# Kernel tuning notes

Hardware: AMD Instinct MI355X
Metric: run time of the kernel (lower is better)

## Reference

```python
import jax, jax.numpy as jnp
import numpy as np

B, S, D, H, E, TOPK = 4, 2048, 1024, 1024, 8, 2

def setup_inputs() -> dict:
    key = jax.random.key(0)
    k1, k2, k3 = jax.random.split(key, 3)
    x = jax.random.normal(k1, (B, S, D), dtype=jnp.float32)
    Wg = jax.random.normal(k2, (D, E), dtype=jnp.float32) * (1.0 / np.sqrt(D))
    bg = jnp.zeros((E,), dtype=jnp.float32)
    We = jax.random.normal(k3, (E, D, H), dtype=jnp.float32) * (1.0 / np.sqrt(D))
    be = jnp.zeros((E, H), dtype=jnp.float32)
    return {"x": x, "Wg": Wg, "bg": bg, "We": We, "be": be, "k": TOPK}

def reference(x, Wg, bg, We, be, k):
    # gate logits: [B, S, E]
    logits = jnp.einsum('bsd,de->bse', x, Wg) + bg
    # top-k gating (values, indices along expert axis)
    top_vals, sel = jax.lax.top_k(logits, k)            # [B, S, k]
    weights = jax.nn.softmax(top_vals.astype(jnp.float32), axis=-1).astype(x.dtype)
    # per-token combine weight for each expert: [B, S, E]
    onehot = jax.nn.one_hot(sel, E, dtype=x.dtype)      # [B, S, k, E]
    comb = jnp.einsum('bsk,bske->bse', weights, onehot)
    # all-expert dense outputs (equivalent math to per-expert gather+GEMM+scatter)
    y = jnp.einsum('bsd,edh->besh', x, We) + be[None, :, None, :]  # [B, E, S, H]
    out = jnp.einsum('bse,besh->bsh', comb, y)          # [B, S, H]
    return out
```

## Files before the change

### kernel.cpp

```cpp
#include <hip/hip_runtime.h>
#include <hip/hip_bf16.h>
#include <hip/hip_fp16.h>

#define NTOK 8192
#define DDIM 1024
#define HDIM 1024
#define NEXP 8

typedef __attribute__((ext_vector_type(8))) short short8;
typedef __attribute__((ext_vector_type(4))) float f32x4;
typedef __attribute__((ext_vector_type(4))) unsigned short us4;

static __device__ __forceinline__ unsigned short f2bf(float f) {
  union { float f; unsigned u; } v; v.f = f;
  return (unsigned short)((v.u + 0x7fffu + ((v.u >> 16) & 1u)) >> 16);
}

static __device__ __forceinline__ void gload16(const void* g, void* l) {
  __builtin_amdgcn_global_load_lds(
      (const __attribute__((address_space(1))) unsigned int*)g,
      (__attribute__((address_space(3))) unsigned int*)l, 16, 0, 0);
}

__global__ __launch_bounds__(256) void gate_kernel(
    const float* __restrict__ x, const float* __restrict__ Wg,
    const float* __restrict__ bg, unsigned short* __restrict__ xb,
    int* __restrict__ sel, float* __restrict__ wts)
{
  const int token = blockIdx.x * 4 + (threadIdx.x >> 6);
  const int lane = threadIdx.x & 63;
  const float* xr = x + (size_t)token * DDIM;

  float acc[NEXP];
#pragma unroll
  for (int e = 0; e < NEXP; ++e) acc[e] = 0.f;

#pragma unroll
  for (int q = 0; q < 4; ++q) {
    const int d0 = q * 256 + lane * 4;
    const float4 xv = *(const float4*)(xr + d0);
    us4 hb;
    hb.x = f2bf(xv.x); hb.y = f2bf(xv.y); hb.z = f2bf(xv.z); hb.w = f2bf(xv.w);
    *(us4*)(xb + (size_t)token * DDIM + d0) = hb;
    const float xs[4] = {xv.x, xv.y, xv.z, xv.w};
#pragma unroll
    for (int j = 0; j < 4; ++j) {
      const float* wr = Wg + (size_t)(d0 + j) * NEXP;
      const float4 wa = *(const float4*)wr;
      const float4 wb = *(const float4*)(wr + 4);
      acc[0] += xs[j] * wa.x; acc[1] += xs[j] * wa.y;
      acc[2] += xs[j] * wa.z; acc[3] += xs[j] * wa.w;
      acc[4] += xs[j] * wb.x; acc[5] += xs[j] * wb.y;
      acc[6] += xs[j] * wb.z; acc[7] += xs[j] * wb.w;
    }
  }

#pragma unroll
  for (int e = 0; e < NEXP; ++e) {
#pragma unroll
    for (int off = 32; off >= 1; off >>= 1)
      acc[e] += __shfl_xor(acc[e], off, 64);
  }

  if (lane == 0) {
    float v[NEXP];
#pragma unroll
    for (int e = 0; e < NEXP; ++e) v[e] = acc[e] + bg[e];
    int i0 = 0; float v0 = v[0];
#pragma unroll
    for (int e = 1; e < NEXP; ++e) if (v[e] > v0) { v0 = v[e]; i0 = e; }
    int i1 = -1; float v1 = -3.4e38f;
#pragma unroll
    for (int e = 0; e < NEXP; ++e) if (e != i0 && v[e] > v1) { v1 = v[e]; i1 = e; }
    const float t = __expf(v1 - v0);
    const float w0 = 1.f / (1.f + t);
    const float w1 = t / (1.f + t);
    sel[token * 2 + 0] = i0;  wts[token * 2 + 0] = w0;
    sel[token * 2 + 1] = i1;  wts[token * 2 + 1] = w1;
  }
}

__global__ __launch_bounds__(256) void route_kernel(
    const int* __restrict__ sel, const float* __restrict__ wts,
    int* __restrict__ counts, int* __restrict__ tlist, float* __restrict__ wlist,
    int* __restrict__ dstrow)
{
  __shared__ int bin[NEXP];
  __shared__ int base[NEXP];
  const int tid = threadIdx.x;
  if (tid < NEXP) bin[tid] = 0;
  __syncthreads();
  const int idx = blockIdx.x * 256 + tid;
  const int e = sel[idx];
  const float w = wts[idx];
  const int rank = atomicAdd(&bin[e], 1);
  __syncthreads();
  if (tid < NEXP) base[tid] = atomicAdd(&counts[tid], bin[tid]);
  __syncthreads();
  const int pos = base[e] + rank;
  tlist[e * NTOK + pos] = idx >> 1;
  wlist[e * NTOK + pos] = w;
  dstrow[e * NTOK + pos] = idx;
}

__global__ __launch_bounds__(256) void transpose_we(
    const float* __restrict__ We, unsigned short* __restrict__ wbt)
{
  const int e = blockIdx.z;
  const int h0 = blockIdx.x * 64;
  const int d0 = blockIdx.y * 64;
  __shared__ float t[64][65];
  const int tx = threadIdx.x;
  const int r0 = tx >> 4;
  const int c0 = (tx & 15) * 4;
  const float* src = We + ((size_t)e * DDIM + d0) * HDIM + h0;
#pragma unroll
  for (int i = 0; i < 4; ++i) {
    const int r = r0 + i * 16;
    const float4 v = *(const float4*)(src + (size_t)r * HDIM + c0);
    t[r][c0] = v.x; t[r][c0 + 1] = v.y; t[r][c0 + 2] = v.z; t[r][c0 + 3] = v.w;
  }
  __syncthreads();
#pragma unroll
  for (int i = 0; i < 4; ++i) {
    const int hr = r0 + i * 16;
    us4 o;
    o.x = f2bf(t[c0][hr]);
    o.y = f2bf(t[c0 + 1][hr]);
    o.z = f2bf(t[c0 + 2][hr]);
    o.w = f2bf(t[c0 + 3][hr]);
    *(us4*)(wbt + ((size_t)e * HDIM + h0 + hr) * DDIM + d0 + c0) = o;
  }
}

__global__ __launch_bounds__(512, 4) void moe_gemm(
    const unsigned short* __restrict__ xb,
    const unsigned short* __restrict__ wbt,
    const float* __restrict__ be,
    const int* __restrict__ counts,
    const int* __restrict__ tlist,
    const float* __restrict__ wlist,
    const int* __restrict__ dstrow,
    __half* __restrict__ yb)
{
  const int e = blockIdx.z;
  const int cnt = counts[e];
  const int tile = blockIdx.y;
  if (tile * 256 >= cnt) return;
  const int n0 = blockIdx.x * 128;

  __shared__ unsigned short As[256 * 64];
  __shared__ unsigned short Bs[128 * 64];

  const int tid = threadIdx.x;
  const int lane = tid & 63;
  const int wv = tid >> 6;
  const int wm = wv >> 1;
  const int wn = wv & 1;

  const int rA = tid >> 3;
  const int kbA = (tid & 7) << 4;
  int aOff[4]; int bOff[2]; int ldsA[4]; int ldsB[2];
#pragma unroll
  for (int q = 0; q < 4; ++q) {
    const int r = q * 64 + rA;
    int trow = tile * 256 + r;
    trow = trow < cnt ? trow : cnt - 1;
    const int tok = tlist[e * NTOK + trow];
    const int kbs = kbA ^ ((r & 7) << 4);
    aOff[q] = tok * DDIM + (kbs >> 1);
    ldsA[q] = r * 64 + (kbA >> 1);
  }
#pragma unroll
  for (int q = 0; q < 2; ++q) {
    const int r = q * 64 + rA;
    const int kbs = kbA ^ ((r & 7) << 4);
    bOff[q] = (e * HDIM + n0 + r) * DDIM + (kbs >> 1);
    ldsB[q] = r * 64 + (kbA >> 1);
  }

  f32x4 acc[4][4];
#pragma unroll
  for (int m = 0; m < 4; ++m)
#pragma unroll
    for (int n = 0; n < 4; ++n)
      acc[m][n] = (f32x4){0.f, 0.f, 0.f, 0.f};

  for (int kt = 0; kt < DDIM / 64; ++kt) {
    __syncthreads();
#pragma unroll
    for (int q = 0; q < 4; ++q) gload16(xb + aOff[q] + kt * 64, &As[ldsA[q]]);
#pragma unroll
    for (int q = 0; q < 2; ++q) gload16(wbt + bOff[q] + kt * 64, &Bs[ldsB[q]]);
    __syncthreads();

#pragma unroll
    for (int kk = 0; kk < 2; ++kk) {
      const int kb = kk * 64 + ((lane >> 4) << 4);
      short8 af[4], bfr[4];
#pragma unroll
      for (int m = 0; m < 4; ++m) {
        const int r = wm * 64 + m * 16 + (lane & 15);
        af[m] = *(const short8*)((const char*)As + r * 128 + (kb ^ ((r & 7) << 4)));
      }
#pragma unroll
      for (int n = 0; n < 4; ++n) {
        const int r = wn * 64 + n * 16 + (lane & 15);
        bfr[n] = *(const short8*)((const char*)Bs + r * 128 + (kb ^ ((r & 7) << 4)));
      }
#pragma unroll
      for (int m = 0; m < 4; ++m)
#pragma unroll
        for (int n = 0; n < 4; ++n)
          acc[m][n] = __builtin_amdgcn_mfma_f32_16x16x32_bf16(af[m], bfr[n], acc[m][n], 0, 0, 0);
    }
  }

  const int rbase = wm * 64 + ((lane >> 4) << 2);
  const int cb = lane & 15;
  float bev[4];
#pragma unroll
  for (int n = 0; n < 4; ++n) bev[n] = be[e * HDIM + n0 + wn * 64 + n * 16 + cb];
#pragma unroll
  for (int m = 0; m < 4; ++m) {
#pragma unroll
    for (int r4 = 0; r4 < 4; ++r4) {
      const int trow = tile * 256 + rbase + m * 16 + r4;
      if (trow < cnt) {
        const int drow = dstrow[e * NTOK + trow];
        const float w = wlist[e * NTOK + trow];
        __half* yrow = yb + (size_t)drow * HDIM + n0 + wn * 64 + cb;
#pragma unroll
        for (int n = 0; n < 4; ++n)
          yrow[n * 16] = __float2half(w * (acc[m][n][r4] + bev[n]));
      }
    }
  }
}

__global__ __launch_bounds__(256) void combine_kernel(
    const __half* __restrict__ yb, float* __restrict__ out)
{
  const int g = blockIdx.x * 256 + threadIdx.x;
  const int tok = g >> 7;
  const int h0 = (g & 127) * 8;
  const short8 p0 = *(const short8*)(yb + ((size_t)tok * 2) * HDIM + h0);
  const short8 p1 = *(const short8*)(yb + ((size_t)tok * 2 + 1) * HDIM + h0);
  float r[8];
#pragma unroll
  for (int j = 0; j < 8; ++j) {
    __half a = *(const __half*)&((const short*)&p0)[j];
    __half b = *(const __half*)&((const short*)&p1)[j];
    r[j] = __half2float(a) + __half2float(b);
  }
  float* o = out + (size_t)tok * HDIM + h0;
  *(float4*)o = (float4){r[0], r[1], r[2], r[3]};
  *(float4*)(o + 4) = (float4){r[4], r[5], r[6], r[7]};
}

extern "C" void kernel_launch(void* const* d_in, const int* in_sizes, int n_in,
                              void* d_out, int out_size, void* d_ws, size_t ws_size,
                              hipStream_t stream)
{
  const float* x  = (const float*)d_in[0];
  const float* Wg = (const float*)d_in[1];
  const float* bg = (const float*)d_in[2];
  const float* We = (const float*)d_in[3];
  const float* be = (const float*)d_in[4];

  char* ws = (char*)d_ws;
  int*   counts = (int*)ws;
  int*   tlist  = (int*)(ws + 256);
  float* wlist  = (float*)(ws + 256 + NEXP * NTOK * 4);
  int*   dstrow = (int*)(ws + 256 + 2 * NEXP * NTOK * 4);
  int*   sel    = (int*)(ws + 256 + 3 * NEXP * NTOK * 4);
  float* wts    = (float*)(ws + 256 + 3 * NEXP * NTOK * 4 + 2 * NTOK * 4);
  unsigned short* xb  = (unsigned short*)(ws + (1 << 21));
  unsigned short* wbt = (unsigned short*)(ws + (1 << 21) + (size_t)NTOK * DDIM * 2);
  __half* yb = (__half*)(ws + (1 << 21) + 2 * (size_t)NTOK * DDIM * 2);
  float* out = (float*)d_out;

  hipMemsetAsync(counts, 0, 256, stream);

  gate_kernel<<<NTOK / 4, 256, 0, stream>>>(x, Wg, bg, xb, sel, wts);
  route_kernel<<<2 * NTOK / 256, 256, 0, stream>>>(sel, wts, counts, tlist, wlist, dstrow);
  transpose_we<<<dim3(HDIM / 64, DDIM / 64, NEXP), 256, 0, stream>>>(We, wbt);
  moe_gemm<<<dim3(HDIM / 128, NTOK / 256, NEXP), 512, 0, stream>>>(
      xb, wbt, be, counts, tlist, wlist, dstrow, yb);
  combine_kernel<<<NTOK * HDIM / 8 / 256, 256, 0, stream>>>(yb, out);
}
```

Measured before the change: 219.5 us.

## Enlarge MoE GEMM tile to 256x256, transpose gate weights, widen We transpose

The expert GEMM block tile grows from 256x128 to 256x256, with 8 waves in a 2x4 layout each computing a 128x64 sub-tile (8x4 MFMA accumulators). This raises arithmetic intensity per LDS load and halves the number of blocks, but doubles accumulator registers and lowers the occupancy hint to 2. Gate weights are pre-transposed into an expert-major layout so each lane reads contiguous float4s per expert. The We transpose now handles 128-row d tiles and writes 16-byte vector stores.

```diff
diff --git a/kernel.cpp b/kernel.cpp
--- a/kernel.cpp
+++ b/kernel.cpp
@@ -10,6 +10,7 @@
 typedef __attribute__((ext_vector_type(8))) short short8;
 typedef __attribute__((ext_vector_type(4))) float f32x4;
 typedef __attribute__((ext_vector_type(4))) unsigned short us4;
+typedef __attribute__((ext_vector_type(8))) unsigned short us8;
 
 static __device__ __forceinline__ unsigned short f2bf(float f) {
   union { float f; unsigned u; } v; v.f = f;
@@ -22,8 +23,16 @@
       (__attribute__((address_space(3))) unsigned int*)l, 16, 0, 0);
 }
 
+__global__ __launch_bounds__(256) void wg_transpose(
+    const float* __restrict__ Wg, float* __restrict__ wgT)
+{
+  const int i = blockIdx.x * 256 + threadIdx.x;
+  const int e = i >> 10, d = i & 1023;
+  wgT[i] = Wg[d * NEXP + e];
+}
+
 __global__ __launch_bounds__(256) void gate_kernel(
-    const float* __restrict__ x, const float* __restrict__ Wg,
+    const float* __restrict__ x, const float* __restrict__ wgT,
     const float* __restrict__ bg, unsigned short* __restrict__ xb,
     int* __restrict__ sel, float* __restrict__ wts)
 {
@@ -42,16 +51,13 @@
     us4 hb;
     hb.x = f2bf(xv.x); hb.y = f2bf(xv.y); hb.z = f2bf(xv.z); hb.w = f2bf(xv.w);
     *(us4*)(xb + (size_t)token * DDIM + d0) = hb;
-    const float xs[4] = {xv.x, xv.y, xv.z, xv.w};
-#pragma unroll
-    for (int j = 0; j < 4; ++j) {
-      const float* wr = Wg + (size_t)(d0 + j) * NEXP;
-      const float4 wa = *(const float4*)wr;
-      const float4 wb = *(const float4*)(wr + 4);
-      acc[0] += xs[j] * wa.x; acc[1] += xs[j] * wa.y;
-      acc[2] += xs[j] * wa.z; acc[3] += xs[j] * wa.w;
-      acc[4] += xs[j] * wb.x; acc[5] += xs[j] * wb.y;
-      acc[6] += xs[j] * wb.z; acc[7] += xs[j] * wb.w;
+#pragma unroll
+    for (int e = 0; e < NEXP; ++e) {
+      const float4 wv = *(const float4*)(wgT + e * DDIM + d0);
+      acc[e] += xv.x * wv.x;
+      acc[e] += xv.y * wv.y;
+      acc[e] += xv.z * wv.z;
+      acc[e] += xv.w * wv.w;
     }
   }
 
@@ -108,32 +114,39 @@
 {
   const int e = blockIdx.z;
   const int h0 = blockIdx.x * 64;
-  const int d0 = blockIdx.y * 64;
-  __shared__ float t[64][65];
+  const int d0 = blockIdx.y * 128;
+  __shared__ float t[128][65];
   const int tx = threadIdx.x;
-  const int r0 = tx >> 4;
-  const int c0 = (tx & 15) * 4;
-  const float* src = We + ((size_t)e * DDIM + d0) * HDIM + h0;
-#pragma unroll
-  for (int i = 0; i < 4; ++i) {
-    const int r = r0 + i * 16;
-    const float4 v = *(const float4*)(src + (size_t)r * HDIM + c0);
-    t[r][c0] = v.x; t[r][c0 + 1] = v.y; t[r][c0 + 2] = v.z; t[r][c0 + 3] = v.w;
+
+  {
+    const int hc = (tx & 15) * 4;
+    const float* src = We + ((size_t)e * DDIM + d0) * HDIM + h0 + hc;
+#pragma unroll
+    for (int i = 0; i < 8; ++i) {
+      const int dr = (tx >> 4) + i * 16;
+      const float4 v = *(const float4*)(src + (size_t)dr * HDIM);
+      t[dr][hc] = v.x; t[dr][hc + 1] = v.y; t[dr][hc + 2] = v.z; t[dr][hc + 3] = v.w;
+    }
   }
   __syncthreads();
-#pragma unroll
-  for (int i = 0; i < 4; ++i) {
-    const int hr = r0 + i * 16;
-    us4 o;
-    o.x = f2bf(t[c0][hr]);
-    o.y = f2bf(t[c0 + 1][hr]);
-    o.z = f2bf(t[c0 + 2][hr]);
-    o.w = f2bf(t[c0 + 3][hr]);
-    *(us4*)(wbt + ((size_t)e * HDIM + h0 + hr) * DDIM + d0 + c0) = o;
-  }
-}
-
-__global__ __launch_bounds__(512, 4) void moe_gemm(
+  {
+    const int dc = (tx & 7) * 16;
+#pragma unroll
+    for (int i2 = 0; i2 < 2; ++i2) {
+      const int hr = (tx >> 3) + i2 * 32;
+      us8 o0, o1;
+#pragma unroll
+      for (int j = 0; j < 8; ++j) ((unsigned short*)&o0)[j] = f2bf(t[dc + j][hr]);
+#pragma unroll
+      for (int j = 0; j < 8; ++j) ((unsigned short*)&o1)[j] = f2bf(t[dc + 8 + j][hr]);
+      unsigned short* dst = wbt + ((size_t)e * HDIM + h0 + hr) * DDIM + d0 + dc;
+      *(us8*)dst = o0;
+      *(us8*)(dst + 8) = o1;
+    }
+  }
+}
+
+__global__ __launch_bounds__(512, 2) void moe_gemm(
     const unsigned short* __restrict__ xb,
     const unsigned short* __restrict__ wbt,
     const float* __restrict__ be,
@@ -147,20 +160,20 @@
   const int cnt = counts[e];
   const int tile = blockIdx.y;
   if (tile * 256 >= cnt) return;
-  const int n0 = blockIdx.x * 128;
+  const int n0 = blockIdx.x * 256;
 
   __shared__ unsigned short As[256 * 64];
-  __shared__ unsigned short Bs[128 * 64];
+  __shared__ unsigned short Bs[256 * 64];
 
   const int tid = threadIdx.x;
   const int lane = tid & 63;
   const int wv = tid >> 6;
-  const int wm = wv >> 1;
-  const int wn = wv & 1;
+  const int wm = wv >> 2;
+  const int wn = wv & 3;
 
   const int rA = tid >> 3;
   const int kbA = (tid & 7) << 4;
-  int aOff[4]; int bOff[2]; int ldsA[4]; int ldsB[2];
+  int aOff[4]; int bOff[4]; int ldsO[4];
 #pragma unroll
   for (int q = 0; q < 4; ++q) {
     const int r = q * 64 + rA;
@@ -169,19 +182,13 @@
     const int tok = tlist[e * NTOK + trow];
     const int kbs = kbA ^ ((r & 7) << 4);
     aOff[q] = tok * DDIM + (kbs >> 1);
-    ldsA[q] = r * 64 + (kbA >> 1);
-  }
-#pragma unroll
-  for (int q = 0; q < 2; ++q) {
-    const int r = q * 64 + rA;
-    const int kbs = kbA ^ ((r & 7) << 4);
     bOff[q] = (e * HDIM + n0 + r) * DDIM + (kbs >> 1);
-    ldsB[q] = r * 64 + (kbA >> 1);
-  }
-
-  f32x4 acc[4][4];
-#pragma unroll
-  for (int m = 0; m < 4; ++m)
+    ldsO[q] = r * 64 + (kbA >> 1);
+  }
+
+  f32x4 acc[8][4];
+#pragma unroll
+  for (int m = 0; m < 8; ++m)
 #pragma unroll
     for (int n = 0; n < 4; ++n)
       acc[m][n] = (f32x4){0.f, 0.f, 0.f, 0.f};
@@ -189,18 +196,18 @@
   for (int kt = 0; kt < DDIM / 64; ++kt) {
     __syncthreads();
 #pragma unroll
-    for (int q = 0; q < 4; ++q) gload16(xb + aOff[q] + kt * 64, &As[ldsA[q]]);
-#pragma unroll
-    for (int q = 0; q < 2; ++q) gload16(wbt + bOff[q] + kt * 64, &Bs[ldsB[q]]);
+    for (int q = 0; q < 4; ++q) gload16(xb + aOff[q] + kt * 64, &As[ldsO[q]]);
+#pragma unroll
+    for (int q = 0; q < 4; ++q) gload16(wbt + bOff[q] + kt * 64, &Bs[ldsO[q]]);
     __syncthreads();
 
 #pragma unroll
     for (int kk = 0; kk < 2; ++kk) {
       const int kb = kk * 64 + ((lane >> 4) << 4);
-      short8 af[4], bfr[4];
-#pragma unroll
-      for (int m = 0; m < 4; ++m) {
-        const int r = wm * 64 + m * 16 + (lane & 15);
+      short8 af[8], bfr[4];
+#pragma unroll
+      for (int m = 0; m < 8; ++m) {
+        const int r = wm * 128 + m * 16 + (lane & 15);
         af[m] = *(const short8*)((const char*)As + r * 128 + (kb ^ ((r & 7) << 4)));
       }
 #pragma unroll
@@ -209,20 +216,20 @@
         bfr[n] = *(const short8*)((const char*)Bs + r * 128 + (kb ^ ((r & 7) << 4)));
       }
 #pragma unroll
-      for (int m = 0; m < 4; ++m)
+      for (int m = 0; m < 8; ++m)
 #pragma unroll
         for (int n = 0; n < 4; ++n)
           acc[m][n] = __builtin_amdgcn_mfma_f32_16x16x32_bf16(af[m], bfr[n], acc[m][n], 0, 0, 0);
     }
   }
 
-  const int rbase = wm * 64 + ((lane >> 4) << 2);
+  const int rbase = wm * 128 + ((lane >> 4) << 2);
   const int cb = lane & 15;
   float bev[4];
 #pragma unroll
   for (int n = 0; n < 4; ++n) bev[n] = be[e * HDIM + n0 + wn * 64 + n * 16 + cb];
 #pragma unroll
-  for (int m = 0; m < 4; ++m) {
+  for (int m = 0; m < 8; ++m) {
 #pragma unroll
     for (int r4 = 0; r4 < 4; ++r4) {
       const int trow = tile * 256 + rbase + m * 16 + r4;
@@ -275,6 +282,7 @@
   int*   dstrow = (int*)(ws + 256 + 2 * NEXP * NTOK * 4);
   int*   sel    = (int*)(ws + 256 + 3 * NEXP * NTOK * 4);
   float* wts    = (float*)(ws + 256 + 3 * NEXP * NTOK * 4 + 2 * NTOK * 4);
+  float* wgT    = (float*)(ws + 0x180000);
   unsigned short* xb  = (unsigned short*)(ws + (1 << 21));
   unsigned short* wbt = (unsigned short*)(ws + (1 << 21) + (size_t)NTOK * DDIM * 2);
   __half* yb = (__half*)(ws + (1 << 21) + 2 * (size_t)NTOK * DDIM * 2);
@@ -282,10 +290,11 @@
 
   hipMemsetAsync(counts, 0, 256, stream);
 
-  gate_kernel<<<NTOK / 4, 256, 0, stream>>>(x, Wg, bg, xb, sel, wts);
+  wg_transpose<<<32, 256, 0, stream>>>(Wg, wgT);
+  gate_kernel<<<NTOK / 4, 256, 0, stream>>>(x, wgT, bg, xb, sel, wts);
   route_kernel<<<2 * NTOK / 256, 256, 0, stream>>>(sel, wts, counts, tlist, wlist, dstrow);
-  transpose_we<<<dim3(HDIM / 64, DDIM / 64, NEXP), 256, 0, stream>>>(We, wbt);
-  moe_gemm<<<dim3(HDIM / 128, NTOK / 256, NEXP), 512, 0, stream>>>(
+  transpose_we<<<dim3(HDIM / 64, DDIM / 128, NEXP), 256, 0, stream>>>(We, wbt);
+  moe_gemm<<<dim3(HDIM / 256, NTOK / 256, NEXP), 512, 0, stream>>>(
       xb, wbt, be, counts, tlist, wlist, dstrow, yb);
   combine_kernel<<<NTOK * HDIM / 8 / 256, 256, 0, stream>>>(yb, out);
 }
```

Result: no change. 222.5 us (+1.4%).
